# Kernel optimization log

Hardware: AMD Instinct MI355X
Metric: run time of the kernel (lower is better)

Reference implementation:

```python
import jax, jax.numpy as jnp
import numpy as np

WIN = 5
EPS = 1e-05


def box_sum(x, win=WIN):
    """3D box-filter window sum, SAME padding (pad=win//2), via separable 1D convs.
    Mathematically identical to F.conv3d(x, ones(1,1,win,win,win), padding=win//2).
    x: [N, C, D, H, W]
    """
    pad = win // 2
    for ax in range(3):  # D, H, W
        kshape = [1, 1, 1, 1, 1]
        kshape[2 + ax] = win
        k = jnp.ones(kshape, x.dtype)
        pads = [(0, 0), (0, 0), (0, 0)]
        pads[ax] = (pad, pad)
        x = jax.lax.conv_general_dilated(
            x, k, window_strides=(1, 1, 1), padding=pads,
            dimension_numbers=('NCDHW', 'OIDHW', 'NCDHW'))
    return x


def setup_inputs() -> dict:
    key = jax.random.key(0)
    k1, k2 = jax.random.split(key)
    shape = (2, 1, 160, 192, 192)
    I = jax.random.normal(k1, shape, dtype=jnp.float32)
    J = jax.random.normal(k2, shape, dtype=jnp.float32)
    return {"I": I, "J": J}


def reference(I, J):
    V = float(WIN ** 3)  # window voxel count
    I_sum = box_sum(I)
    J_sum = box_sum(J)
    I2_sum = box_sum(I * I)
    J2_sum = box_sum(J * J)
    IJ_sum = box_sum(I * J)

    u_I = I_sum / V
    u_J = J_sum / V
    cross = IJ_sum - u_J * I_sum - u_I * J_sum + u_I * u_J * V
    I_var = I2_sum - 2.0 * u_I * I_sum + u_I * u_I * V
    J_var = J2_sum - 2.0 * u_J * J_sum + u_J * u_J * V
    cc = cross * cross / (I_var * J_var + EPS)
    # single channel: avg over channels is identity; loss = -mean(cc)
    return -1.0 * jnp.mean(cc)
```

## Files before the change

### kernel.cpp

```cpp
#include <hip/hip_runtime.h>


namespace {
constexpr int Wd = 192, Hd = 192, Dd = 160;
constexpr int SH = 192;
constexpr int SD = 192 * 192;
constexpr long SN = (long)SD * Dd;
constexpr int CD = 6;
constexpr int NCHUNK = 27;
constexpr int TROW = 72;
constexpr int TILEF = 2 * 20 * TROW;
constexpr float INV_V = 1.0f / 125.0f;
constexpr float EPSf = 1e-5f;

__device__ __forceinline__ void wslide(const float h[8], float o[4]) {
  float s0 = h[0] + h[1] + h[2] + h[3] + h[4];
  float s1 = s0 - h[0] + h[5];
  float s2 = s1 - h[1] + h[6];
  float s3 = s2 - h[2] + h[7];
  o[0] = s0; o[1] = s1; o[2] = s2; o[3] = s3;
}

__device__ __forceinline__ void gl_lds16(const float* g, float* l) {
  __builtin_amdgcn_global_load_lds(
      (const __attribute__((address_space(1))) void*)g,
      (__attribute__((address_space(3))) void*)l, 16, 0, 0);
}
}

__global__ __launch_bounds__(256) void ncc_fused(const float* __restrict__ I,
                                                 const float* __restrict__ Jv,
                                                 float* __restrict__ out) {
  __shared__ float tile[2][TILEF];
  __shared__ float red[4];

  const int tid = threadIdx.x;
  const int tx = tid & 15;
  const int ty = tid >> 4;
  const int wbase = blockIdx.x * 64;
  const int hbase = blockIdx.y * 16;
  const int n  = blockIdx.z / NCHUNK;
  const int d_lo = (blockIdx.z % NCHUNK) * CD;

  const float* Ib = I  + (long)n * SN;
  const float* Jb = Jv + (long)n * SN;

  const int wave = tid >> 6, lane = tid & 63;
  const int arr = wave >> 1;
  const float* gsrc = arr ? Jb : Ib;
  int goff[3]; int loff[3]; bool on[3];
  #pragma unroll
  for (int r = 0; r < 3; ++r) {
    const int seg = wave * 180 + r * 64 + lane;
    on[r] = (r < 2) || (lane < 52);
    const int rem = seg - arr * 360;
    const int row = rem / 18, c16 = rem % 18;
    const int hh = hbase + row - 2;
    const int hc = min(max(hh, 0), Hd - 1);
    const int gw = wbase - 2 + c16 * 4;
    const int gc = min(max(gw, 0), Wd - 4);
    goff[r] = hc * SH + gc;
    loff[r] = seg * 4;
  }

  {
    const int s0 = d_lo - 2;
    if (s0 >= 0 && s0 < Dd) {
      const float* base = gsrc + (long)s0 * SD;
      #pragma unroll
      for (int r = 0; r < 3; ++r) if (on[r]) gl_lds16(base + goff[r], &tile[0][loff[r]]);
    }
  }
  __syncthreads();

  const bool fixl = (wbase == 0)   && (tx == 0);
  const bool fixr = (wbase == 128) && (tx == 15);

  float ring[5][5][4];
  float acc = 0.0f;

  constexpr int T = CD + 4;
  for (int t0 = 0; t0 < T; t0 += 5) {
    #pragma unroll
    for (int p = 0; p < 5; ++p) {
      const int t = t0 + p;
      const int s = d_lo - 2 + t;

      {
        const int sn = s + 1;
        if ((t + 1) < T && sn >= 0 && sn < Dd) {
          const float* base = gsrc + (long)sn * SD;
          float* dst = &tile[(t + 1) & 1][0];
          #pragma unroll
          for (int r = 0; r < 3; ++r) if (on[r]) gl_lds16(base + goff[r], dst + loff[r]);
        }
      }

      float hsI[8], hsJ[8], hsII[8], hsJJ[8], hsIJ[8];
      #pragma unroll
      for (int c = 0; c < 8; ++c) {
        hsI[c] = 0.f; hsJ[c] = 0.f; hsII[c] = 0.f; hsJJ[c] = 0.f; hsIJ[c] = 0.f;
      }
      if (s >= 0 && s < Dd) {
        const float* bufc = &tile[t & 1][0];
        #pragma unroll
        for (int dh = 0; dh < 5; ++dh) {
          const int rrow = ty + dh;
          const int hh = hbase + rrow - 2;
          if (hh >= 0 && hh < Hd) {
            const float* pa = bufc + rrow * TROW + 4 * tx;
            const float* pb = pa + 20 * TROW;
            float a[8], b[8];
            ((float4*)a)[0] = ((const float4*)pa)[0];
            ((float4*)a)[1] = ((const float4*)pa)[1];
            ((float4*)b)[0] = ((const float4*)pb)[0];
            ((float4*)b)[1] = ((const float4*)pb)[1];
            if (fixl) { a[2]=a[0]; a[3]=a[1]; a[0]=0.f; a[1]=0.f;
                        b[2]=b[0]; b[3]=b[1]; b[0]=0.f; b[1]=0.f; }
            if (fixr) { a[4]=a[6]; a[5]=a[7]; a[6]=0.f; a[7]=0.f;
                        b[4]=b[6]; b[5]=b[7]; b[6]=0.f; b[7]=0.f; }
            #pragma unroll
            for (int c = 0; c < 8; ++c) {
              const float x = a[c], y = b[c];
              hsI[c]  += x;
              hsJ[c]  += y;
              hsII[c] = fmaf(x, x, hsII[c]);
              hsJJ[c] = fmaf(y, y, hsJJ[c]);
              hsIJ[c] = fmaf(x, y, hsIJ[c]);
            }
          }
        }
      }

      wslide(hsI,  ring[p][0]);
      wslide(hsJ,  ring[p][1]);
      wslide(hsII, ring[p][2]);
      wslide(hsJJ, ring[p][3]);
      wslide(hsIJ, ring[p][4]);

      const int d = d_lo + t - 4;
      if (t >= 4 && d < Dd) {
        #pragma unroll
        for (int k = 0; k < 4; ++k) {
          float SI = 0.f, SJ = 0.f, SII = 0.f, SJJ = 0.f, SIJ = 0.f;
          #pragma unroll
          for (int q = 0; q < 5; ++q) {
            SI  += ring[q][0][k];
            SJ  += ring[q][1][k];
            SII += ring[q][2][k];
            SJJ += ring[q][3][k];
            SIJ += ring[q][4][k];
          }
          const float cross = SIJ - SI * SJ * INV_V;
          const float vI    = SII - SI * SI * INV_V;
          const float vJ    = SJJ - SJ * SJ * INV_V;
          acc += cross * cross / (vI * vJ + EPSf);
        }
      }

      __syncthreads();
    }
  }

  #pragma unroll
  for (int off = 32; off > 0; off >>= 1) acc += __shfl_xor(acc, off, 64);
  if ((tid & 63) == 0) red[tid >> 6] = acc;
  __syncthreads();
  if (tid == 0) {
    const float total = red[0] + red[1] + red[2] + red[3];
    atomicAdd(out, total * (-1.0f / 11796480.0f));
  }
}

extern "C" void kernel_launch(void* const* d_in, const int* in_sizes, int n_in,
                              void* d_out, int out_size, void* d_ws, size_t ws_size,
                              hipStream_t stream) {
  const float* I = (const float*)d_in[0];
  const float* J = (const float*)d_in[1];
  float* out = (float*)d_out;
  hipMemsetAsync(out, 0, sizeof(float), stream);
  dim3 grid(3, 12, 2 * NCHUNK);
  ncc_fused<<<grid, 256, 0, stream>>>(I, J, out);
}
```

Measured before the change: 165.6 us.

## Triple-buffer depth slices with two-ahead async prefetch and partial vmcnt waits

```diff
diff --git a/kernel.cpp b/kernel.cpp
--- a/kernel.cpp
+++ b/kernel.cpp
@@ -31,7 +31,7 @@
 __global__ __launch_bounds__(256) void ncc_fused(const float* __restrict__ I,
                                                  const float* __restrict__ Jv,
                                                  float* __restrict__ out) {
-  __shared__ float tile[2][TILEF];
+  __shared__ float tile[3][TILEF];
   __shared__ float red[4];
 
   const int tid = threadIdx.x;
@@ -63,15 +63,18 @@
     loff[r] = seg * 4;
   }
 
-  {
-    const int s0 = d_lo - 2;
-    if (s0 >= 0 && s0 < Dd) {
-      const float* base = gsrc + (long)s0 * SD;
-      #pragma unroll
-      for (int r = 0; r < 3; ++r) if (on[r]) gl_lds16(base + goff[r], &tile[0][loff[r]]);
-    }
+  if (d_lo > 0) {
+    const float* b0 = gsrc + (long)(d_lo - 2) * SD;
+    const float* b1 = gsrc + (long)(d_lo - 1) * SD;
+    #pragma unroll
+    for (int r = 0; r < 3; ++r) if (on[r]) gl_lds16(b0 + goff[r], &tile[0][loff[r]]);
+    #pragma unroll
+    for (int r = 0; r < 3; ++r) if (on[r]) gl_lds16(b1 + goff[r], &tile[1][loff[r]]);
+    asm volatile("s_waitcnt vmcnt(3) lgkmcnt(0)" ::: "memory");
+  } else {
+    asm volatile("s_waitcnt vmcnt(0) lgkmcnt(0)" ::: "memory");
   }
-  __syncthreads();
+  __builtin_amdgcn_s_barrier();
 
   const bool fixl = (wbase == 0)   && (tx == 0);
   const bool fixr = (wbase == 128) && (tx == 15);
@@ -80,86 +83,84 @@
   float acc = 0.0f;
 
   constexpr int T = CD + 4;
-  for (int t0 = 0; t0 < T; t0 += 5) {
+  #pragma unroll
+  for (int t = 0; t < T; ++t) {
+    const int p = t % 5;
+    const int s = d_lo - 2 + t;
+
+    const bool issue = ((t + 2) < T) && ((d_lo + t) < Dd);
+    if (issue) {
+      const float* base = gsrc + (long)(d_lo + t) * SD;
+      float* dst = &tile[(t + 2) % 3][0];
+      #pragma unroll
+      for (int r = 0; r < 3; ++r) if (on[r]) gl_lds16(base + goff[r], dst + loff[r]);
+    }
+
+    float hsI[8], hsJ[8], hsII[8], hsJJ[8], hsIJ[8];
     #pragma unroll
-    for (int p = 0; p < 5; ++p) {
-      const int t = t0 + p;
-      const int s = d_lo - 2 + t;
-
-      {
-        const int sn = s + 1;
-        if ((t + 1) < T && sn >= 0 && sn < Dd) {
-          const float* base = gsrc + (long)sn * SD;
-          float* dst = &tile[(t + 1) & 1][0];
+    for (int c = 0; c < 8; ++c) {
+      hsI[c] = 0.f; hsJ[c] = 0.f; hsII[c] = 0.f; hsJJ[c] = 0.f; hsIJ[c] = 0.f;
+    }
+    if (s >= 0 && s < Dd) {
+      const float* bufc = &tile[t % 3][0];
+      #pragma unroll
+      for (int dh = 0; dh < 5; ++dh) {
+        const int rrow = ty + dh;
+        const int hh = hbase + rrow - 2;
+        if (hh >= 0 && hh < Hd) {
+          const float* pa = bufc + rrow * TROW + 4 * tx;
+          const float* pb = pa + 20 * TROW;
+          float a[8], b[8];
+          ((float4*)a)[0] = ((const float4*)pa)[0];
+          ((float4*)a)[1] = ((const float4*)pa)[1];
+          ((float4*)b)[0] = ((const float4*)pb)[0];
+          ((float4*)b)[1] = ((const float4*)pb)[1];
+          if (fixl) { a[2]=a[0]; a[3]=a[1]; a[0]=0.f; a[1]=0.f;
+                      b[2]=b[0]; b[3]=b[1]; b[0]=0.f; b[1]=0.f; }
+          if (fixr) { a[4]=a[6]; a[5]=a[7]; a[6]=0.f; a[7]=0.f;
+                      b[4]=b[6]; b[5]=b[7]; b[6]=0.f; b[7]=0.f; }
           #pragma unroll
-          for (int r = 0; r < 3; ++r) if (on[r]) gl_lds16(base + goff[r], dst + loff[r]);
-        }
-      }
-
-      float hsI[8], hsJ[8], hsII[8], hsJJ[8], hsIJ[8];
-      #pragma unroll
-      for (int c = 0; c < 8; ++c) {
-        hsI[c] = 0.f; hsJ[c] = 0.f; hsII[c] = 0.f; hsJJ[c] = 0.f; hsIJ[c] = 0.f;
-      }
-      if (s >= 0 && s < Dd) {
-        const float* bufc = &tile[t & 1][0];
-        #pragma unroll
-        for (int dh = 0; dh < 5; ++dh) {
-          const int rrow = ty + dh;
-          const int hh = hbase + rrow - 2;
-          if (hh >= 0 && hh < Hd) {
-            const float* pa = bufc + rrow * TROW + 4 * tx;
-            const float* pb = pa + 20 * TROW;
-            float a[8], b[8];
-            ((float4*)a)[0] = ((const float4*)pa)[0];
-            ((float4*)a)[1] = ((const float4*)pa)[1];
-            ((float4*)b)[0] = ((const float4*)pb)[0];
-            ((float4*)b)[1] = ((const float4*)pb)[1];
-            if (fixl) { a[2]=a[0]; a[3]=a[1]; a[0]=0.f; a[1]=0.f;
-                        b[2]=b[0]; b[3]=b[1]; b[0]=0.f; b[1]=0.f; }
-            if (fixr) { a[4]=a[6]; a[5]=a[7]; a[6]=0.f; a[7]=0.f;
-                        b[4]=b[6]; b[5]=b[7]; b[6]=0.f; b[7]=0.f; }
-            #pragma unroll
-            for (int c = 0; c < 8; ++c) {
-              const float x = a[c], y = b[c];
-              hsI[c]  += x;
-              hsJ[c]  += y;
-              hsII[c] = fmaf(x, x, hsII[c]);
-              hsJJ[c] = fmaf(y, y, hsJJ[c]);
-              hsIJ[c] = fmaf(x, y, hsIJ[c]);
-            }
+          for (int c = 0; c < 8; ++c) {
+            const float x = a[c], y = b[c];
+            hsI[c]  += x;
+            hsJ[c]  += y;
+            hsII[c] = fmaf(x, x, hsII[c]);
+            hsJJ[c] = fmaf(y, y, hsJJ[c]);
+            hsIJ[c] = fmaf(x, y, hsIJ[c]);
           }
         }
       }
+    }
 
-      wslide(hsI,  ring[p][0]);
-      wslide(hsJ,  ring[p][1]);
-      wslide(hsII, ring[p][2]);
-      wslide(hsJJ, ring[p][3]);
-      wslide(hsIJ, ring[p][4]);
+    wslide(hsI,  ring[p][0]);
+    wslide(hsJ,  ring[p][1]);
+    wslide(hsII, ring[p][2]);
+    wslide(hsJJ, ring[p][3]);
+    wslide(hsIJ, ring[p][4]);
 
-      const int d = d_lo + t - 4;
-      if (t >= 4 && d < Dd) {
+    const int d = d_lo + t - 4;
+    if (t >= 4 && d < Dd) {
+      #pragma unroll
+      for (int k = 0; k < 4; ++k) {
+        float SI = 0.f, SJ = 0.f, SII = 0.f, SJJ = 0.f, SIJ = 0.f;
         #pragma unroll
-        for (int k = 0; k < 4; ++k) {
-          float SI = 0.f, SJ = 0.f, SII = 0.f, SJJ = 0.f, SIJ = 0.f;
-          #pragma unroll
-          for (int q = 0; q < 5; ++q) {
-            SI  += ring[q][0][k];
-            SJ  += ring[q][1][k];
-            SII += ring[q][2][k];
-            SJJ += ring[q][3][k];
-            SIJ += ring[q][4][k];
-          }
-          const float cross = SIJ - SI * SJ * INV_V;
-          const float vI    = SII - SI * SI * INV_V;
-          const float vJ    = SJJ - SJ * SJ * INV_V;
-          acc += cross * cross / (vI * vJ + EPSf);
+        for (int q = 0; q < 5; ++q) {
+          SI  += ring[q][0][k];
+          SJ  += ring[q][1][k];
+          SII += ring[q][2][k];
+          SJJ += ring[q][3][k];
+          SIJ += ring[q][4][k];
         }
+        const float cross = SIJ - SI * SJ * INV_V;
+        const float vI    = SII - SI * SI * INV_V;
+        const float vJ    = SJJ - SJ * SJ * INV_V;
+        acc += cross * cross / (vI * vJ + EPSf);
       }
+    }
 
-      __syncthreads();
-    }
+    if (issue) asm volatile("s_waitcnt vmcnt(3) lgkmcnt(0)" ::: "memory");
+    else       asm volatile("s_waitcnt vmcnt(0) lgkmcnt(0)" ::: "memory");
+    __builtin_amdgcn_s_barrier();
   }
 
   #pragma unroll
```

Measured after the change: 214.8 us. 29.7% more time.
